# Kernel optimization log

Hardware: AMD Instinct MI355X
Metric: run time of the kernel (lower is better)

Reference implementation:

```python
import jax, jax.numpy as jnp
import numpy as np

B = 8192          # batch
IN = 4096         # in_features
OUT = 4096        # out_features
BS = 64           # block_size
NBR = OUT // BS   # block rows = 64
NBC = IN // BS    # block cols = 64
BPR = 16


def setup_inputs() -> dict:
    key = jax.random.key(0)
    k1, k2, k3 = jax.random.split(key, 3)
    x = jax.random.normal(k1, (B, IN), dtype=jnp.float32)
    values = jax.random.normal(k2, (NBR * BPR, BS, BS), dtype=jnp.float32) * 0.02
    bias = jax.random.normal(k3, (OUT,), dtype=jnp.float32) * 0.02
    # static BSR pattern: per block-row, BPR sorted unique block-column indices
    rng = np.random.default_rng(0)
    cols = np.stack([np.sort(rng.choice(NBC, BPR, replace=False)) for _ in range(NBR)])
    col_indices = jnp.asarray(cols.reshape(-1), dtype=jnp.int32)  # [NBR*BPR]
    return {"x": x, "values": values, "bias": bias, "col_indices": col_indices}


def reference(x, values, bias, col_indices):
    # y = (A_bsr @ x.T).T + bias  ==  x @ A.T + bias, with A in BSR layout.
    xb = x.reshape(B, NBC, BS)                       # [B, nbc, bs] block columns of x
    cols = col_indices.reshape(NBR, BPR)             # [nbr, j]
    xg = xb[:, cols, :]                              # [B, nbr, j, bs] gathered input blocks
    vals = values.reshape(NBR, BPR, BS, BS)          # [nbr, j, bs_out, bs_in]
    out = jnp.einsum('rjob,Brjb->Bro', vals, xg)     # block-sparse GEMM
    return out.reshape(B, OUT) + bias
```

## Files before the change

### kernel.cpp

```cpp
#include <hip/hip_runtime.h>
#include <hip/hip_bf16.h>
#include <stdint.h>

#define B_DIM   8192
#define IN_DIM  4096
#define OUT_DIM 4096
#define BSZ     64
#define NBR_    64
#define BPR_    16
#define KTOT    1024
#define MT      256
#define BKK     32

typedef __attribute__((ext_vector_type(4))) float  floatx4;
typedef __attribute__((ext_vector_type(8))) short  shortx8;
typedef __attribute__((ext_vector_type(4))) float  fragc;

__device__ __forceinline__ unsigned short f2bf(float f) {
  __bf16 b = (__bf16)f;
  return __builtin_bit_cast(unsigned short, b);
}

__device__ __forceinline__ void gload_lds16(const void* g, void* l) {
  __builtin_amdgcn_global_load_lds(
      (const __attribute__((address_space(1))) unsigned int*)g,
      (__attribute__((address_space(3))) unsigned int*)l, 16, 0, 0);
}

__global__ __launch_bounds__(256) void cvt_kernel(const float* __restrict__ src,
                                                  unsigned short* __restrict__ dst,
                                                  int n8) {
  const int stride = gridDim.x * blockDim.x;
  for (int i = blockIdx.x * blockDim.x + threadIdx.x; i < n8; i += stride) {
    floatx4 a = ((const floatx4*)src)[2 * i];
    floatx4 b = ((const floatx4*)src)[2 * i + 1];
    uint4 o;
    o.x = (unsigned int)f2bf(a.x) | ((unsigned int)f2bf(a.y) << 16);
    o.y = (unsigned int)f2bf(a.z) | ((unsigned int)f2bf(a.w) << 16);
    o.z = (unsigned int)f2bf(b.x) | ((unsigned int)f2bf(b.y) << 16);
    o.w = (unsigned int)f2bf(b.z) | ((unsigned int)f2bf(b.w) << 16);
    ((uint4*)dst)[i] = o;
  }
}

template <bool PRECONV>
__global__ __launch_bounds__(256, 3)
void bsr_gemm(const void* __restrict__ xin, const void* __restrict__ vin,
              const float* __restrict__ bias, const int* __restrict__ colidx,
              float* __restrict__ out) {
  const int r  = blockIdx.x;
  const int m0 = blockIdx.y * MT;
  const int tid  = threadIdx.x;
  const int wave = tid >> 6;
  const int lane = tid & 63;
  const int l16  = lane & 15;
  const int quad = lane >> 4;

  __shared__ __align__(16) unsigned short As[MT * BKK];
  __shared__ __align__(16) unsigned short Bs[BSZ * BKK];
  __shared__ int scols[BPR_];

  if (tid < BPR_) scols[tid] = colidx[r * BPR_ + tid];

  fragc acc[4][4] = {};

  __syncthreads();

  for (int ks = 0; ks < KTOT / BKK; ++ks) {
    const int jb  = ks >> 1;
    const int kb0 = (ks & 1) * BKK;
    const int colbase = scols[jb] * BSZ + kb0;

    __syncthreads();

    if constexpr (PRECONV) {
      const unsigned short* xb = (const unsigned short*)xin;
      const unsigned short* vb = (const unsigned short*)vin;
      const int sub = lane >> 2;
      const int kc  = (lane & 3) * 8;
      #pragma unroll
      for (int i = 0; i < 4; ++i) {
        const int row = wave * 64 + i * 16 + sub;
        gload_lds16(xb + (size_t)(m0 + row) * IN_DIM + colbase + kc,
                    &As[(wave * 64 + i * 16) * BKK]);
      }
      gload_lds16(vb + ((size_t)(r * BPR_ + jb) * BSZ + wave * 16 + sub) * BSZ + kb0 + kc,
                  &Bs[(wave * 16) * BKK]);
    } else {
      const float* x = (const float*)xin;
      const float* v = (const float*)vin;
      const int arow = tid >> 3;
      const int acol = (tid & 7) * 4;
      #pragma unroll
      for (int i = 0; i < 8; ++i) {
        const int row = i * 32 + arow;
        floatx4 f = *(const floatx4*)&x[(size_t)(m0 + row) * IN_DIM + colbase + acol];
        uint2 p;
        p.x = (unsigned int)f2bf(f.x) | ((unsigned int)f2bf(f.y) << 16);
        p.y = (unsigned int)f2bf(f.z) | ((unsigned int)f2bf(f.w) << 16);
        *(uint2*)&As[row * BKK + acol] = p;
      }
      #pragma unroll
      for (int i = 0; i < 2; ++i) {
        const int row = i * 32 + arow;
        floatx4 f = *(const floatx4*)&v[((size_t)(r * BPR_ + jb) * BSZ + row) * BSZ + kb0 + acol];
        uint2 p;
        p.x = (unsigned int)f2bf(f.x) | ((unsigned int)f2bf(f.y) << 16);
        p.y = (unsigned int)f2bf(f.z) | ((unsigned int)f2bf(f.w) << 16);
        *(uint2*)&Bs[row * BKK + acol] = p;
      }
    }

    __syncthreads();

    shortx8 af[4], bfv[4];
    #pragma unroll
    for (int mi = 0; mi < 4; ++mi)
      af[mi] = *(const shortx8*)&As[(wave * 64 + mi * 16 + l16) * BKK + quad * 8];
    #pragma unroll
    for (int ni = 0; ni < 4; ++ni)
      bfv[ni] = *(const shortx8*)&Bs[(ni * 16 + l16) * BKK + quad * 8];
    #pragma unroll
    for (int mi = 0; mi < 4; ++mi) {
      #pragma unroll
      for (int ni = 0; ni < 4; ++ni)
        acc[mi][ni] = __builtin_amdgcn_mfma_f32_16x16x32_bf16(af[mi], bfv[ni],
                                                              acc[mi][ni], 0, 0, 0);
    }
  }

  #pragma unroll
  for (int ni = 0; ni < 4; ++ni) {
    const int col = r * BSZ + ni * 16 + l16;
    const float bv = bias[col];
    #pragma unroll
    for (int mi = 0; mi < 4; ++mi) {
      #pragma unroll
      for (int reg = 0; reg < 4; ++reg) {
        const int row = m0 + wave * 64 + mi * 16 + quad * 4 + reg;
        out[(size_t)row * OUT_DIM + col] = acc[mi][ni][reg] + bv;
      }
    }
  }
}

extern "C" void kernel_launch(void* const* d_in, const int* in_sizes, int n_in,
                              void* d_out, int out_size, void* d_ws, size_t ws_size,
                              hipStream_t stream) {
  const float* x    = (const float*)d_in[0];
  const float* vals = (const float*)d_in[1];
  const float* bias = (const float*)d_in[2];
  const int*   cols = (const int*)d_in[3];
  float* out = (float*)d_out;

  const size_t x_elems = (size_t)B_DIM * IN_DIM;
  const size_t v_elems = (size_t)NBR_ * BPR_ * BSZ * BSZ;
  const size_t xb_bytes = x_elems * sizeof(unsigned short);
  const size_t vb_bytes = v_elems * sizeof(unsigned short);

  dim3 grid(NBR_, B_DIM / MT);

  if (ws_size >= xb_bytes + vb_bytes) {
    unsigned short* xb = (unsigned short*)d_ws;
    unsigned short* vb = (unsigned short*)((char*)d_ws + xb_bytes);
    cvt_kernel<<<dim3(8192), dim3(256), 0, stream>>>(x, xb, (int)(x_elems / 8));
    cvt_kernel<<<dim3(2048), dim3(256), 0, stream>>>(vals, vb, (int)(v_elems / 8));
    bsr_gemm<true><<<grid, dim3(256), 0, stream>>>(xb, vb, bias, cols, out);
  } else {
    bsr_gemm<false><<<grid, dim3(256), 0, stream>>>(x, vals, bias, cols, out);
  }
}
```

Baseline: 404.4 us.

## Load MFMA fragments directly from global memory with register double buffering

Removes the LDS staging and block-wide barriers from the block-sparse GEMM. Each wave now loads its A and B bf16 fragments straight from global memory into registers, double-buffered across k-steps so loads overlap the MFMAs. Column indices are held in registers, and the fp32 fallback path is replaced by a simple naive kernel. In exchange, the four waves no longer share the weight tile through LDS, so each wave fetches it separately, the A loads are uncoalesced 16-byte row reads, and register pressure is higher.

After: 483.8 us. 19.6% more time.

```diff
diff --git a/kernel.cpp b/kernel.cpp
--- a/kernel.cpp
+++ b/kernel.cpp
@@ -21,12 +21,6 @@
   return __builtin_bit_cast(unsigned short, b);
 }
 
-__device__ __forceinline__ void gload_lds16(const void* g, void* l) {
-  __builtin_amdgcn_global_load_lds(
-      (const __attribute__((address_space(1))) unsigned int*)g,
-      (__attribute__((address_space(3))) unsigned int*)l, 16, 0, 0);
-}
-
 __global__ __launch_bounds__(256) void cvt_kernel(const float* __restrict__ src,
                                                   unsigned short* __restrict__ dst,
                                                   int n8) {
@@ -43,9 +37,9 @@
   }
 }
 
-template <bool PRECONV>
-__global__ __launch_bounds__(256, 3)
-void bsr_gemm(const void* __restrict__ xin, const void* __restrict__ vin,
+__global__ __launch_bounds__(256)
+void bsr_gemm(const unsigned short* __restrict__ xb,
+              const unsigned short* __restrict__ vb,
               const float* __restrict__ bias, const int* __restrict__ colidx,
               float* __restrict__ out) {
   const int r  = blockIdx.x;
@@ -56,78 +50,51 @@
   const int l16  = lane & 15;
   const int quad = lane >> 4;
 
-  __shared__ __align__(16) unsigned short As[MT * BKK];
-  __shared__ __align__(16) unsigned short Bs[BSZ * BKK];
-  __shared__ int scols[BPR_];
+  int cidx[BPR_];
+  #pragma unroll
+  for (int j = 0; j < BPR_; ++j) cidx[j] = colidx[r * BPR_ + j];
 
-  if (tid < BPR_) scols[tid] = colidx[r * BPR_ + tid];
+  const unsigned short* xrow = xb + (size_t)(m0 + wave * 64 + l16) * IN_DIM + quad * 8;
+  const unsigned short* vblk = vb + ((size_t)(r * BPR_) * BSZ + l16) * BSZ + quad * 8;
 
   fragc acc[4][4] = {};
+  shortx8 a0[4], b0[4], a1[4], b1[4];
 
-  __syncthreads();
+#define LD(ks, af, bf)                                                        \
+  {                                                                           \
+    const int jb_ = (ks) >> 1, kb0_ = ((ks) & 1) * BKK;                       \
+    const unsigned short* ap = xrow + cidx[jb_] * BSZ + kb0_;                 \
+    _Pragma("unroll")                                                         \
+    for (int mi = 0; mi < 4; ++mi)                                            \
+      af[mi] = *(const shortx8*)(ap + (size_t)mi * 16 * IN_DIM);              \
+    const unsigned short* bp = vblk + (size_t)jb_ * BSZ * BSZ + kb0_;         \
+    _Pragma("unroll")                                                         \
+    for (int ni = 0; ni < 4; ++ni)                                            \
+      bf[ni] = *(const shortx8*)(bp + ni * 16 * BSZ);                         \
+  }
 
-  for (int ks = 0; ks < KTOT / BKK; ++ks) {
-    const int jb  = ks >> 1;
-    const int kb0 = (ks & 1) * BKK;
-    const int colbase = scols[jb] * BSZ + kb0;
+#define MM(af, bf)                                                            \
+  {                                                                           \
+    _Pragma("unroll")                                                         \
+    for (int mi = 0; mi < 4; ++mi) {                                          \
+      _Pragma("unroll")                                                       \
+      for (int ni = 0; ni < 4; ++ni)                                          \
+        acc[mi][ni] = __builtin_amdgcn_mfma_f32_16x16x32_bf16(af[mi], bf[ni], \
+                                                              acc[mi][ni],    \
+                                                              0, 0, 0);       \
+    }                                                                         \
+  }
 
-    __syncthreads();
-
-    if constexpr (PRECONV) {
-      const unsigned short* xb = (const unsigned short*)xin;
-      const unsigned short* vb = (const unsigned short*)vin;
-      const int sub = lane >> 2;
-      const int kc  = (lane & 3) * 8;
-      #pragma unroll
-      for (int i = 0; i < 4; ++i) {
-        const int row = wave * 64 + i * 16 + sub;
-        gload_lds16(xb + (size_t)(m0 + row) * IN_DIM + colbase + kc,
-                    &As[(wave * 64 + i * 16) * BKK]);
-      }
-      gload_lds16(vb + ((size_t)(r * BPR_ + jb) * BSZ + wave * 16 + sub) * BSZ + kb0 + kc,
-                  &Bs[(wave * 16) * BKK]);
-    } else {
-      const float* x = (const float*)xin;
-      const float* v = (const float*)vin;
-      const int arow = tid >> 3;
-      const int acol = (tid & 7) * 4;
-      #pragma unroll
-      for (int i = 0; i < 8; ++i) {
-        const int row = i * 32 + arow;
-        floatx4 f = *(const floatx4*)&x[(size_t)(m0 + row) * IN_DIM + colbase + acol];
-        uint2 p;
-        p.x = (unsigned int)f2bf(f.x) | ((unsigned int)f2bf(f.y) << 16);
-        p.y = (unsigned int)f2bf(f.z) | ((unsigned int)f2bf(f.w) << 16);
-        *(uint2*)&As[row * BKK + acol] = p;
-      }
-      #pragma unroll
-      for (int i = 0; i < 2; ++i) {
-        const int row = i * 32 + arow;
-        floatx4 f = *(const floatx4*)&v[((size_t)(r * BPR_ + jb) * BSZ + row) * BSZ + kb0 + acol];
-        uint2 p;
-        p.x = (unsigned int)f2bf(f.x) | ((unsigned int)f2bf(f.y) << 16);
-        p.y = (unsigned int)f2bf(f.z) | ((unsigned int)f2bf(f.w) << 16);
-        *(uint2*)&Bs[row * BKK + acol] = p;
-      }
-    }
-
-    __syncthreads();
-
-    shortx8 af[4], bfv[4];
-    #pragma unroll
-    for (int mi = 0; mi < 4; ++mi)
-      af[mi] = *(const shortx8*)&As[(wave * 64 + mi * 16 + l16) * BKK + quad * 8];
-    #pragma unroll
-    for (int ni = 0; ni < 4; ++ni)
-      bfv[ni] = *(const shortx8*)&Bs[(ni * 16 + l16) * BKK + quad * 8];
-    #pragma unroll
-    for (int mi = 0; mi < 4; ++mi) {
-      #pragma unroll
-      for (int ni = 0; ni < 4; ++ni)
-        acc[mi][ni] = __builtin_amdgcn_mfma_f32_16x16x32_bf16(af[mi], bfv[ni],
-                                                              acc[mi][ni], 0, 0, 0);
-    }
+  LD(0, a0, b0);
+  #pragma unroll
+  for (int ks = 0; ks < KTOT / BKK; ks += 2) {
+    LD(ks + 1, a1, b1);
+    MM(a0, b0);
+    if (ks + 2 < KTOT / BKK) LD(ks + 2, a0, b0);
+    MM(a1, b1);
   }
+#undef LD
+#undef MM
 
   #pragma unroll
   for (int ni = 0; ni < 4; ++ni) {
@@ -144,6 +111,25 @@
   }
 }
 
+__global__ __launch_bounds__(256)
+void bsr_naive(const float* __restrict__ x, const float* __restrict__ v,
+               const float* __restrict__ bias, const int* __restrict__ colidx,
+               float* __restrict__ out) {
+  const size_t gid = (size_t)blockIdx.x * blockDim.x + threadIdx.x;
+  if (gid >= (size_t)B_DIM * OUT_DIM) return;
+  const int b = gid / OUT_DIM;
+  const int oc = gid % OUT_DIM;
+  const int rr = oc / BSZ, o = oc % BSZ;
+  float s = bias[oc];
+  for (int j = 0; j < BPR_; ++j) {
+    const int c = colidx[rr * BPR_ + j];
+    const float* xp = x + (size_t)b * IN_DIM + c * BSZ;
+    const float* vp = v + ((size_t)(rr * BPR_ + j) * BSZ + o) * BSZ;
+    for (int k = 0; k < BSZ; ++k) s += vp[k] * xp[k];
+  }
+  out[gid] = s;
+}
+
 extern "C" void kernel_launch(void* const* d_in, const int* in_sizes, int n_in,
                               void* d_out, int out_size, void* d_ws, size_t ws_size,
                               hipStream_t stream) {
@@ -158,15 +144,16 @@
   const size_t xb_bytes = x_elems * sizeof(unsigned short);
   const size_t vb_bytes = v_elems * sizeof(unsigned short);
 
-  dim3 grid(NBR_, B_DIM / MT);
-
   if (ws_size >= xb_bytes + vb_bytes) {
-    unsigned short* xb = (unsigned short*)d_ws;
-    unsigned short* vb = (unsigned short*)((char*)d_ws + xb_bytes);
-    cvt_kernel<<<dim3(8192), dim3(256), 0, stream>>>(x, xb, (int)(x_elems / 8));
-    cvt_kernel<<<dim3(2048), dim3(256), 0, stream>>>(vals, vb, (int)(v_elems / 8));
-    bsr_gemm<true><<<grid, dim3(256), 0, stream>>>(xb, vb, bias, cols, out);
+    unsigned short* xbp = (unsigned short*)d_ws;
+    unsigned short* vbp = (unsigned short*)((char*)d_ws + xb_bytes);
+    cvt_kernel<<<dim3(8192), dim3(256), 0, stream>>>(x, xbp, (int)(x_elems / 8));
+    cvt_kernel<<<dim3(2048), dim3(256), 0, stream>>>(vals, vbp, (int)(v_elems / 8));
+    dim3 grid(NBR_, B_DIM / MT);
+    bsr_gemm<<<grid, dim3(256), 0, stream>>>(xbp, vbp, bias, cols, out);
   } else {
-    bsr_gemm<false><<<grid, dim3(256), 0, stream>>>(x, vals, bias, cols, out);
+    const size_t n = (size_t)B_DIM * OUT_DIM;
+    bsr_naive<<<dim3((unsigned)((n + 255) / 256)), dim3(256), 0, stream>>>(
+        x, vals, bias, cols, out);
   }
 }
```
